# Performance work log

Measured on AMD Instinct MI355X. Metric: run time of the kernel, lower is better.

Reference implementation:

```python
import jax, jax.numpy as jnp
import numpy as np

N_ATOMS = 100_000
N_PAIRS = 6_400_000
CUTOFF = 5.0
CUTON = 4.0


def setup_inputs() -> dict:
    key = jax.random.key(0)
    k = jax.random.split(key, 4)
    atomic_numbers = jax.random.uniform(k[0], (N_ATOMS,), jnp.float32, 1.0, 94.0)
    displacements = jax.random.normal(k[1], (N_PAIRS, 3), jnp.float32) * 2.0
    idx_i = jnp.sort(jax.random.randint(k[2], (N_PAIRS,), 0, N_ATOMS, jnp.int32))
    idx_j = jax.random.randint(k[3], (N_PAIRS,), 0, N_ATOMS, jnp.int32)
    atom_mask = jnp.ones((N_ATOMS,), jnp.float32)
    batch_segments = jnp.zeros((N_ATOMS,), jnp.int32)
    batch_mask = jnp.ones((N_PAIRS,), jnp.float32)
    # ZBL parameters (non-trainable constants from setup())
    a_coefficient = jnp.asarray(0.8854, jnp.float32)
    a_exponent = jnp.asarray(0.23, jnp.float32)
    phi_coefficients = jnp.array([0.18175, 0.50986, 0.28022, 0.02817], jnp.float32)
    phi_exponents = jnp.array([3.1998, 0.94229, 0.4029, 0.20162], jnp.float32)
    return dict(
        atomic_numbers=atomic_numbers,
        displacements=displacements,
        idx_i=idx_i,
        idx_j=idx_j,
        atom_mask=atom_mask,
        batch_segments=batch_segments,
        batch_mask=batch_mask,
        batch_size=1,
        a_coefficient=a_coefficient,
        a_exponent=a_exponent,
        phi_coefficients=phi_coefficients,
        phi_exponents=phi_exponents,
    )


def _switch_fn(distances):
    # smooth 1 -> 0 switch between CUTON and CUTOFF
    x = (CUTOFF - distances) / (CUTOFF - CUTON)
    poly = ((6.0 * x - 15.0) * x + 10.0) * x ** 3
    return jnp.where(distances < CUTON, 1.0, jnp.where(distances >= CUTOFF, 0.0, poly))


def reference(atomic_numbers, displacements, idx_i, idx_j, atom_mask,
              batch_segments, batch_mask, batch_size,
              a_coefficient, a_exponent, phi_coefficients, phi_exponents):
    distances = jnp.maximum(jnp.linalg.norm(displacements, axis=-1), 1e-10)  # [E]
    switch_off = _switch_fn(distances)

    za = jnp.power(atomic_numbers, jnp.abs(a_exponent))  # [N]
    denominator = jnp.maximum(za[idx_i] + za[idx_j], 1e-10)  # [E]
    a_ij = jnp.abs(a_coefficient) / denominator
    arguments = distances / a_ij  # [E]

    coefficients = jax.nn.softmax(jnp.abs(phi_coefficients))  # [4]
    exponents = jnp.abs(phi_exponents)  # [4]
    log_terms = -exponents[None, :] * arguments[:, None]  # [E,4]
    max_log = jnp.max(log_terms, axis=1, keepdims=True)
    # NOTE: faithful to the original -- max_log is never added back
    phi = jnp.sum(coefficients[None, :] * jnp.exp(log_terms - max_log), axis=1)  # [E]

    log_repulsion = (jnp.log(0.5)
                     + jnp.log(atomic_numbers[idx_i])
                     + jnp.log(atomic_numbers[idx_j])
                     - jnp.log(distances)
                     + jnp.log(jnp.maximum(phi, 1e-30))
                     + jnp.log(jnp.maximum(switch_off, 1e-30)))
    repulsion = jnp.exp(log_repulsion) * batch_mask  # [E]

    Erep = jax.ops.segment_sum(repulsion, segment_ids=idx_i,
                               num_segments=atomic_numbers.shape[0])  # [N]
    Erep = Erep * atom_mask
    return Erep[..., None, None, None]
```

## Files before the change

kernel.cpp:

```cpp
#include <hip/hip_runtime.h>
#include <math.h>

#define LOG2E 1.4426950408889634f


__global__ __launch_bounds__(256) void zbl_prep_kernel(
    const float* __restrict__ z, const float* __restrict__ a_coef,
    const float* __restrict__ a_exp, const float* __restrict__ phi_c,
    const float* __restrict__ phi_e, float2* __restrict__ tab,
    float* __restrict__ out, float* __restrict__ consts, int n_atoms) {
  int n = blockIdx.x * blockDim.x + threadIdx.x;
  if (n < n_atoms) {
    float zi = z[n];
    float ae = fabsf(a_exp[0]);
    float za = __builtin_amdgcn_exp2f(ae * __builtin_amdgcn_logf(zi));
    tab[n] = make_float2(zi, za);
    out[n] = 0.0f;
  }
  if (blockIdx.x == 0 && threadIdx.x == 0) {
    float c[4], e2[4];
    float m = -1e30f;
    for (int k = 0; k < 4; ++k) { c[k] = fabsf(phi_c[k]); m = fmaxf(m, c[k]); }
    float s = 0.0f;
    for (int k = 0; k < 4; ++k) { c[k] = expf(c[k] - m); s += c[k]; }
    for (int k = 0; k < 4; ++k) c[k] /= s;
    int kmin = 0;
    for (int k = 0; k < 4; ++k) {
      e2[k] = fabsf(phi_e[k]) * LOG2E;
      if (e2[k] < e2[kmin]) kmin = k;
    }
    float inv_a = 1.0f / fabsf(a_coef[0]);
    consts[0] = c[kmin];
    int p = 1;
    for (int k = 0; k < 4; ++k) {
      if (k != kmin) {
        consts[p] = c[k];
        consts[3 + p] = (e2[k] - e2[kmin]) * inv_a;
        ++p;
      }
    }
  }
}

__global__ __launch_bounds__(256) void zbl_edge_kernel(
    const float* __restrict__ disp, const int* __restrict__ idx_i,
    const int* __restrict__ idx_j, const float* __restrict__ bmask,
    const float2* __restrict__ tab, const float* __restrict__ consts,
    const float* __restrict__ amask, float* __restrict__ out, int n_edges) {
  const int lane = threadIdx.x & 63;
  const long wave = (long)blockIdx.x * (blockDim.x >> 6) + (threadIdx.x >> 6);
  const long base = wave * 256;

  const float c0 = consts[0], c1 = consts[1], c2 = consts[2], c3 = consts[3];
  const float dd1 = consts[4], dd2 = consts[5], dd3 = consts[6];

  #pragma unroll
  for (int c = 0; c < 4; ++c) {
    const long e = base + (long)(c << 6) + lane;
    int key = -1;
    float v = 0.0f;
    if (e < (long)n_edges) {
      const int i = idx_i[e];
      const int j = idx_j[e];
      const float dx = disp[3 * e + 0];
      const float dy = disp[3 * e + 1];
      const float dz = disp[3 * e + 2];
      float n2 = fmaxf(dx * dx + dy * dy + dz * dz, 1e-20f);
      float r = __builtin_amdgcn_rsqf(n2);
      float d = n2 * r;
      float x = 5.0f - d;
      float poly = ((6.0f * x - 15.0f) * x + 10.0f) * x * x * x;
      float sw = (d < 4.0f) ? 1.0f : ((d >= 5.0f) ? 0.0f : poly);
      float2 ti = tab[i];
      float2 tj = tab[j];
      float q = d * fmaxf(ti.y + tj.y, 1e-10f);
      float phi = c0 + c1 * __builtin_amdgcn_exp2f(-dd1 * q)
                     + c2 * __builtin_amdgcn_exp2f(-dd2 * q)
                     + c3 * __builtin_amdgcn_exp2f(-dd3 * q);
      v = 0.5f * ti.x * tj.x * r * fmaxf(phi, 1e-30f) *
          fmaxf(sw, 1e-30f) * bmask[e];
      key = i;
    }

    #pragma unroll
    for (int off = 1; off < 64; off <<= 1) {
      float v2 = __shfl_down(v, off, 64);
      int k2 = __shfl_down(key, off, 64);
      if (lane + off < 64 && k2 == key) v += v2;
    }
    int kup = __shfl_up(key, 1, 64);
    if (key >= 0 && (lane == 0 || kup != key))
      atomicAdd(&out[key], v * amask[key]);
  }
}

extern "C" void kernel_launch(void* const* d_in, const int* in_sizes, int n_in,
                              void* d_out, int out_size, void* d_ws,
                              size_t ws_size, hipStream_t stream) {
  const float* atomic_numbers = (const float*)d_in[0];
  const float* disp           = (const float*)d_in[1];
  const int*   idx_i          = (const int*)d_in[2];
  const int*   idx_j          = (const int*)d_in[3];
  const float* atom_mask      = (const float*)d_in[4];
  const float* bmask          = (const float*)d_in[6];
  const float* a_coef         = (const float*)d_in[8];
  const float* a_exp          = (const float*)d_in[9];
  const float* phi_c          = (const float*)d_in[10];
  const float* phi_e          = (const float*)d_in[11];

  int n_atoms = in_sizes[0];
  int n_edges = in_sizes[2];

  float* out = (float*)d_out;
  float2* tab = (float2*)d_ws;
  float* consts = (float*)((char*)d_ws + (size_t)n_atoms * sizeof(float2));

  int atom_blocks = (n_atoms + 255) / 256;
  long waves = ((long)n_edges + 255) / 256;
  int edge_blocks = (int)((waves + 3) / 4);

  zbl_prep_kernel<<<atom_blocks, 256, 0, stream>>>(
      atomic_numbers, a_coef, a_exp, phi_c, phi_e, tab, out, consts, n_atoms);
  zbl_edge_kernel<<<edge_blocks, 256, 0, stream>>>(
      disp, idx_i, idx_j, bmask, tab, consts, atom_mask, out, n_edges);
}
```

Measured before the change: 53.58 us.

## Vectorize edge loads and aggregate segment sums in shared-memory slots

```diff
diff --git a/kernel.cpp b/kernel.cpp
--- a/kernel.cpp
+++ b/kernel.cpp
@@ -2,6 +2,8 @@
 #include <math.h>
 
 #define LOG2E 1.4426950408889634f
+#define NSLOT 512
+#define EPB   1024
 
 
 __global__ __launch_bounds__(256) void zbl_prep_kernel(
@@ -42,55 +44,101 @@
   }
 }
 
+__device__ __forceinline__ void zbl_edge_compute(
+    float dx, float dy, float dz, int i, int j, float bm,
+    const float2* __restrict__ tab, float c0, float c1, float c2, float c3,
+    float dd1, float dd2, float dd3, int& kk, float& vv) {
+  float n2 = fmaxf(dx * dx + dy * dy + dz * dz, 1e-20f);
+  float r = __builtin_amdgcn_rsqf(n2);
+  float d = n2 * r;
+  float x = 5.0f - d;
+  float poly = ((6.0f * x - 15.0f) * x + 10.0f) * x * x * x;
+  float sw = (d < 4.0f) ? 1.0f : ((d >= 5.0f) ? 0.0f : poly);
+  float2 ti = tab[i];
+  float2 tj = tab[j];
+  float q = d * fmaxf(ti.y + tj.y, 1e-10f);
+  float phi = c0 + c1 * __builtin_amdgcn_exp2f(-dd1 * q)
+                 + c2 * __builtin_amdgcn_exp2f(-dd2 * q)
+                 + c3 * __builtin_amdgcn_exp2f(-dd3 * q);
+  vv = 0.5f * ti.x * tj.x * r * fmaxf(phi, 1e-30f) * fmaxf(sw, 1e-30f) * bm;
+  kk = i;
+}
+
 __global__ __launch_bounds__(256) void zbl_edge_kernel(
     const float* __restrict__ disp, const int* __restrict__ idx_i,
     const int* __restrict__ idx_j, const float* __restrict__ bmask,
     const float2* __restrict__ tab, const float* __restrict__ consts,
     const float* __restrict__ amask, float* __restrict__ out, int n_edges) {
-  const int lane = threadIdx.x & 63;
-  const long wave = (long)blockIdx.x * (blockDim.x >> 6) + (threadIdx.x >> 6);
-  const long base = wave * 256;
+  __shared__ float acc[NSLOT];
+  const int t = threadIdx.x;
+  const long block_base = (long)blockIdx.x * EPB;
 
+  acc[t] = 0.0f;
+  acc[t + 256] = 0.0f;
+
+  const int key_base = idx_i[block_base];
   const float c0 = consts[0], c1 = consts[1], c2 = consts[2], c3 = consts[3];
   const float dd1 = consts[4], dd2 = consts[5], dd3 = consts[6];
 
+  const long L = (long)blockIdx.x * 256 + t;
+  const long e0 = L * 4;
+
+  int k[4] = {-1, -1, -1, -1};
+  float v[4] = {0.f, 0.f, 0.f, 0.f};
+
+  if (e0 + 3 < (long)n_edges) {
+    const float4* d4 = (const float4*)disp;
+    float4 A = d4[3 * L], B = d4[3 * L + 1], Cc = d4[3 * L + 2];
+    int4 I = ((const int4*)idx_i)[L];
+    int4 J = ((const int4*)idx_j)[L];
+    float4 BM = ((const float4*)bmask)[L];
+    zbl_edge_compute(A.x, A.y, A.z, I.x, J.x, BM.x, tab, c0, c1, c2, c3, dd1, dd2, dd3, k[0], v[0]);
+    zbl_edge_compute(A.w, B.x, B.y, I.y, J.y, BM.y, tab, c0, c1, c2, c3, dd1, dd2, dd3, k[1], v[1]);
+    zbl_edge_compute(B.z, B.w, Cc.x, I.z, J.z, BM.z, tab, c0, c1, c2, c3, dd1, dd2, dd3, k[2], v[2]);
+    zbl_edge_compute(Cc.y, Cc.z, Cc.w, I.w, J.w, BM.w, tab, c0, c1, c2, c3, dd1, dd2, dd3, k[3], v[3]);
+  } else {
+    #pragma unroll
+    for (int m = 0; m < 4; ++m) {
+      const long e = e0 + m;
+      if (e < (long)n_edges)
+        zbl_edge_compute(disp[3 * e], disp[3 * e + 1], disp[3 * e + 2],
+                         idx_i[e], idx_j[e], bmask[e], tab, c0, c1, c2, c3,
+                         dd1, dd2, dd3, k[m], v[m]);
+    }
+  }
+
+  __syncthreads();
+
+  auto flush = [&](int key, float s) {
+    if (key < 0) return;
+    int slot = key - key_base;
+    if ((unsigned)slot < (unsigned)NSLOT) atomicAdd(&acc[slot], s);
+    else atomicAdd(&out[key], s * amask[key]);
+  };
+
+  int cur = k[0];
+  float s = v[0];
   #pragma unroll
-  for (int c = 0; c < 4; ++c) {
-    const long e = base + (long)(c << 6) + lane;
-    int key = -1;
-    float v = 0.0f;
-    if (e < (long)n_edges) {
-      const int i = idx_i[e];
-      const int j = idx_j[e];
-      const float dx = disp[3 * e + 0];
-      const float dy = disp[3 * e + 1];
-      const float dz = disp[3 * e + 2];
-      float n2 = fmaxf(dx * dx + dy * dy + dz * dz, 1e-20f);
-      float r = __builtin_amdgcn_rsqf(n2);
-      float d = n2 * r;
-      float x = 5.0f - d;
-      float poly = ((6.0f * x - 15.0f) * x + 10.0f) * x * x * x;
-      float sw = (d < 4.0f) ? 1.0f : ((d >= 5.0f) ? 0.0f : poly);
-      float2 ti = tab[i];
-      float2 tj = tab[j];
-      float q = d * fmaxf(ti.y + tj.y, 1e-10f);
-      float phi = c0 + c1 * __builtin_amdgcn_exp2f(-dd1 * q)
-                     + c2 * __builtin_amdgcn_exp2f(-dd2 * q)
-                     + c3 * __builtin_amdgcn_exp2f(-dd3 * q);
-      v = 0.5f * ti.x * tj.x * r * fmaxf(phi, 1e-30f) *
-          fmaxf(sw, 1e-30f) * bmask[e];
-      key = i;
+  for (int m = 1; m < 4; ++m) {
+    if (k[m] == cur) {
+      s += v[m];
+    } else {
+      flush(cur, s);
+      cur = k[m];
+      s = v[m];
     }
+  }
+  flush(cur, s);
 
-    #pragma unroll
-    for (int off = 1; off < 64; off <<= 1) {
-      float v2 = __shfl_down(v, off, 64);
-      int k2 = __shfl_down(key, off, 64);
-      if (lane + off < 64 && k2 == key) v += v2;
+  __syncthreads();
+
+  #pragma unroll
+  for (int s2 = 0; s2 < NSLOT; s2 += 256) {
+    float val = acc[t + s2];
+    if (val != 0.0f) {
+      int a = key_base + t + s2;
+      atomicAdd(&out[a], val * amask[a]);
     }
-    int kup = __shfl_up(key, 1, 64);
-    if (key >= 0 && (lane == 0 || kup != key))
-      atomicAdd(&out[key], v * amask[key]);
   }
 }
 
@@ -116,8 +164,7 @@
   float* consts = (float*)((char*)d_ws + (size_t)n_atoms * sizeof(float2));
 
   int atom_blocks = (n_atoms + 255) / 256;
-  long waves = ((long)n_edges + 255) / 256;
-  int edge_blocks = (int)((waves + 3) / 4);
+  int edge_blocks = (int)(((long)n_edges + EPB - 1) / EPB);
 
   zbl_prep_kernel<<<atom_blocks, 256, 0, stream>>>(
       atomic_numbers, a_coef, a_exp, phi_c, phi_e, tab, out, consts, n_atoms);
```

Result: faster. 47.43 us (median of 2 runs) (-11.5%).

## Fuse prep into edge kernel with shared-memory segment accumulation per block

Applied to the files above, without the earlier changes.

```diff
diff --git a/kernel.cpp b/kernel.cpp
--- a/kernel.cpp
+++ b/kernel.cpp
@@ -2,95 +2,151 @@
 #include <math.h>
 
 #define LOG2E 1.4426950408889634f
+#define NSLOT 512
+#define EPT   8
+#define EPB   (256 * EPT)
 
+__global__ __launch_bounds__(256, 6) void zbl_fused_kernel(
+    const float* __restrict__ z, const float* __restrict__ amask,
+    const float* __restrict__ disp, const int* __restrict__ idx_i,
+    const int* __restrict__ idx_j, const float* __restrict__ bmask,
+    const float* __restrict__ a_coef, const float* __restrict__ a_exp,
+    const float* __restrict__ phi_c, const float* __restrict__ phi_e,
+    float* __restrict__ out, int n_edges, int n_atoms) {
+  __shared__ float za_s[NSLOT];
+  __shared__ float acc[NSLOT];
+  const int t = threadIdx.x;
+  const long bb = (long)blockIdx.x * EPB;
+  const long Q = (long)blockIdx.x * 256 + t;
+  const long e0 = Q * (long)EPT;
 
-__global__ __launch_bounds__(256) void zbl_prep_kernel(
-    const float* __restrict__ z, const float* __restrict__ a_coef,
-    const float* __restrict__ a_exp, const float* __restrict__ phi_c,
-    const float* __restrict__ phi_e, float2* __restrict__ tab,
-    float* __restrict__ out, float* __restrict__ consts, int n_atoms) {
-  int n = blockIdx.x * blockDim.x + threadIdx.x;
-  if (n < n_atoms) {
-    float zi = z[n];
-    float ae = fabsf(a_exp[0]);
-    float za = __builtin_amdgcn_exp2f(ae * __builtin_amdgcn_logf(zi));
-    tab[n] = make_float2(zi, za);
-    out[n] = 0.0f;
+  const float ae = fabsf(a_exp[0]);
+  const float inv_a = 1.0f / fabsf(a_coef[0]);
+  float cc0 = fabsf(phi_c[0]), cc1 = fabsf(phi_c[1]);
+  float cc2 = fabsf(phi_c[2]), cc3 = fabsf(phi_c[3]);
+  {
+    float mx = fmaxf(fmaxf(cc0, cc1), fmaxf(cc2, cc3));
+    cc0 = expf(cc0 - mx); cc1 = expf(cc1 - mx);
+    cc2 = expf(cc2 - mx); cc3 = expf(cc3 - mx);
+    float inv_s = 1.0f / (cc0 + cc1 + cc2 + cc3);
+    cc0 *= inv_s; cc1 *= inv_s; cc2 *= inv_s; cc3 *= inv_s;
   }
-  if (blockIdx.x == 0 && threadIdx.x == 0) {
-    float c[4], e2[4];
-    float m = -1e30f;
-    for (int k = 0; k < 4; ++k) { c[k] = fabsf(phi_c[k]); m = fmaxf(m, c[k]); }
-    float s = 0.0f;
-    for (int k = 0; k < 4; ++k) { c[k] = expf(c[k] - m); s += c[k]; }
-    for (int k = 0; k < 4; ++k) c[k] /= s;
-    int kmin = 0;
-    for (int k = 0; k < 4; ++k) {
-      e2[k] = fabsf(phi_e[k]) * LOG2E;
-      if (e2[k] < e2[kmin]) kmin = k;
-    }
-    float inv_a = 1.0f / fabsf(a_coef[0]);
-    consts[0] = c[kmin];
-    int p = 1;
-    for (int k = 0; k < 4; ++k) {
-      if (k != kmin) {
-        consts[p] = c[k];
-        consts[3 + p] = (e2[k] - e2[kmin]) * inv_a;
-        ++p;
+  float q0 = fabsf(phi_e[0]) * LOG2E, q1 = fabsf(phi_e[1]) * LOG2E;
+  float q2 = fabsf(phi_e[2]) * LOG2E, q3 = fabsf(phi_e[3]) * LOG2E;
+  const float emin = fminf(fminf(q0, q1), fminf(q2, q3));
+  const float dd0 = (q0 - emin) * inv_a, dd1 = (q1 - emin) * inv_a;
+  const float dd2 = (q2 - emin) * inv_a, dd3 = (q3 - emin) * inv_a;
+
+  const int key_base = idx_i[bb];
+  const int a0 = min(key_base + t, n_atoms - 1);
+  const int a1 = min(key_base + t + 256, n_atoms - 1);
+  const float zw0 = z[a0], zw1 = z[a1];
+  const float am0 = amask[a0], am1 = amask[a1];
+
+  int kk[EPT];
+  float dx[EPT], dy[EPT], dz[EPT], bm[EPT], zj[EPT];
+  #pragma unroll
+  for (int m = 0; m < EPT; ++m) { kk[m] = -1; dx[m] = dy[m] = dz[m] = bm[m] = 0.f; zj[m] = 1.f; }
+
+  if (e0 + (EPT - 1) < (long)n_edges) {
+    int4 I0 = ((const int4*)idx_i)[2 * Q];
+    int4 I1 = ((const int4*)idx_i)[2 * Q + 1];
+    int4 J0 = ((const int4*)idx_j)[2 * Q];
+    int4 J1 = ((const int4*)idx_j)[2 * Q + 1];
+    const float4* d4 = (const float4*)disp;
+    float4 D0 = d4[6 * Q + 0], D1 = d4[6 * Q + 1], D2 = d4[6 * Q + 2];
+    float4 D3 = d4[6 * Q + 3], D4 = d4[6 * Q + 4], D5 = d4[6 * Q + 5];
+    float4 B0 = ((const float4*)bmask)[2 * Q];
+    float4 B1 = ((const float4*)bmask)[2 * Q + 1];
+    zj[0] = z[J0.x]; zj[1] = z[J0.y]; zj[2] = z[J0.z]; zj[3] = z[J0.w];
+    zj[4] = z[J1.x]; zj[5] = z[J1.y]; zj[6] = z[J1.z]; zj[7] = z[J1.w];
+    kk[0] = I0.x; kk[1] = I0.y; kk[2] = I0.z; kk[3] = I0.w;
+    kk[4] = I1.x; kk[5] = I1.y; kk[6] = I1.z; kk[7] = I1.w;
+    dx[0] = D0.x; dy[0] = D0.y; dz[0] = D0.z;
+    dx[1] = D0.w; dy[1] = D1.x; dz[1] = D1.y;
+    dx[2] = D1.z; dy[2] = D1.w; dz[2] = D2.x;
+    dx[3] = D2.y; dy[3] = D2.z; dz[3] = D2.w;
+    dx[4] = D3.x; dy[4] = D3.y; dz[4] = D3.z;
+    dx[5] = D3.w; dy[5] = D4.x; dz[5] = D4.y;
+    dx[6] = D4.z; dy[6] = D4.w; dz[6] = D5.x;
+    dx[7] = D5.y; dy[7] = D5.z; dz[7] = D5.w;
+    bm[0] = B0.x; bm[1] = B0.y; bm[2] = B0.z; bm[3] = B0.w;
+    bm[4] = B1.x; bm[5] = B1.y; bm[6] = B1.z; bm[7] = B1.w;
+  } else {
+    #pragma unroll
+    for (int m = 0; m < EPT; ++m) {
+      const long e = e0 + m;
+      if (e < (long)n_edges) {
+        kk[m] = idx_i[e];
+        zj[m] = z[idx_j[e]];
+        dx[m] = disp[3 * e]; dy[m] = disp[3 * e + 1]; dz[m] = disp[3 * e + 2];
+        bm[m] = bmask[e];
       }
     }
   }
-}
 
-__global__ __launch_bounds__(256) void zbl_edge_kernel(
-    const float* __restrict__ disp, const int* __restrict__ idx_i,
-    const int* __restrict__ idx_j, const float* __restrict__ bmask,
-    const float2* __restrict__ tab, const float* __restrict__ consts,
-    const float* __restrict__ amask, float* __restrict__ out, int n_edges) {
-  const int lane = threadIdx.x & 63;
-  const long wave = (long)blockIdx.x * (blockDim.x >> 6) + (threadIdx.x >> 6);
-  const long base = wave * 256;
+  acc[t] = 0.0f;
+  acc[t + 256] = 0.0f;
+  za_s[t] = __builtin_amdgcn_exp2f(ae * __builtin_amdgcn_logf(zw0));
+  za_s[t + 256] = __builtin_amdgcn_exp2f(ae * __builtin_amdgcn_logf(zw1));
+  const float fi0 = 0.5f * zw0 * am0;
+  const float fi1 = 0.5f * zw1 * am1;
+  __syncthreads();
 
-  const float c0 = consts[0], c1 = consts[1], c2 = consts[2], c3 = consts[3];
-  const float dd1 = consts[4], dd2 = consts[5], dd3 = consts[6];
+  float vv[EPT];
+  #pragma unroll
+  for (int m = 0; m < EPT; ++m) {
+    float za_i;
+    {
+      int s = kk[m] - key_base;
+      if ((unsigned)s < (unsigned)NSLOT) za_i = za_s[s];
+      else if (kk[m] >= 0)
+        za_i = __builtin_amdgcn_exp2f(ae * __builtin_amdgcn_logf(z[kk[m]]));
+      else za_i = 0.0f;
+    }
+    float n2 = fmaxf(dx[m] * dx[m] + dy[m] * dy[m] + dz[m] * dz[m], 1e-20f);
+    float r = __builtin_amdgcn_rsqf(n2);
+    float d = n2 * r;
+    float x = 5.0f - d;
+    float poly = ((6.0f * x - 15.0f) * x + 10.0f) * x * x * x;
+    float sw = (d < 4.0f) ? 1.0f : ((d >= 5.0f) ? 0.0f : poly);
+    float zaj = __builtin_amdgcn_exp2f(ae * __builtin_amdgcn_logf(zj[m]));
+    float qq = d * fmaxf(za_i + zaj, 1e-10f);
+    float phi = cc0 * __builtin_amdgcn_exp2f(-dd0 * qq)
+              + cc1 * __builtin_amdgcn_exp2f(-dd1 * qq)
+              + cc2 * __builtin_amdgcn_exp2f(-dd2 * qq)
+              + cc3 * __builtin_amdgcn_exp2f(-dd3 * qq);
+    vv[m] = zj[m] * r * fmaxf(phi, 1e-30f) * fmaxf(sw, 1e-30f) * bm[m];
+  }
 
-  #pragma unroll
-  for (int c = 0; c < 4; ++c) {
-    const long e = base + (long)(c << 6) + lane;
-    int key = -1;
-    float v = 0.0f;
-    if (e < (long)n_edges) {
-      const int i = idx_i[e];
-      const int j = idx_j[e];
-      const float dx = disp[3 * e + 0];
-      const float dy = disp[3 * e + 1];
-      const float dz = disp[3 * e + 2];
-      float n2 = fmaxf(dx * dx + dy * dy + dz * dz, 1e-20f);
-      float r = __builtin_amdgcn_rsqf(n2);
-      float d = n2 * r;
-      float x = 5.0f - d;
-      float poly = ((6.0f * x - 15.0f) * x + 10.0f) * x * x * x;
-      float sw = (d < 4.0f) ? 1.0f : ((d >= 5.0f) ? 0.0f : poly);
-      float2 ti = tab[i];
-      float2 tj = tab[j];
-      float q = d * fmaxf(ti.y + tj.y, 1e-10f);
-      float phi = c0 + c1 * __builtin_amdgcn_exp2f(-dd1 * q)
-                     + c2 * __builtin_amdgcn_exp2f(-dd2 * q)
-                     + c3 * __builtin_amdgcn_exp2f(-dd3 * q);
-      v = 0.5f * ti.x * tj.x * r * fmaxf(phi, 1e-30f) *
-          fmaxf(sw, 1e-30f) * bmask[e];
-      key = i;
+  auto flush = [&](int key, float s) {
+    if (key < 0) return;
+    int slot = key - key_base;
+    if ((unsigned)slot < (unsigned)NSLOT) {
+      atomicAdd(&acc[slot], s);
+    } else {
+      atomicAdd(&out[key], s * 0.5f * z[key] * amask[key]);
     }
+  };
 
+  {
+    int cur = kk[0];
+    float s = vv[0];
     #pragma unroll
-    for (int off = 1; off < 64; off <<= 1) {
-      float v2 = __shfl_down(v, off, 64);
-      int k2 = __shfl_down(key, off, 64);
-      if (lane + off < 64 && k2 == key) v += v2;
+    for (int m = 1; m < EPT; ++m) {
+      if (kk[m] == cur) s += vv[m];
+      else { flush(cur, s); cur = kk[m]; s = vv[m]; }
     }
-    int kup = __shfl_up(key, 1, 64);
-    if (key >= 0 && (lane == 0 || kup != key))
-      atomicAdd(&out[key], v * amask[key]);
+    flush(cur, s);
+  }
+
+  __syncthreads();
+
+  {
+    float val = acc[t];
+    if (val != 0.0f) atomicAdd(&out[key_base + t], val * fi0);
+    val = acc[t + 256];
+    if (val != 0.0f) atomicAdd(&out[key_base + t + 256], val * fi1);
   }
 }
 
@@ -112,15 +168,11 @@
   int n_edges = in_sizes[2];
 
   float* out = (float*)d_out;
-  float2* tab = (float2*)d_ws;
-  float* consts = (float*)((char*)d_ws + (size_t)n_atoms * sizeof(float2));
 
-  int atom_blocks = (n_atoms + 255) / 256;
-  long waves = ((long)n_edges + 255) / 256;
-  int edge_blocks = (int)((waves + 3) / 4);
+  hipMemsetAsync(out, 0, (size_t)out_size * sizeof(float), stream);
 
-  zbl_prep_kernel<<<atom_blocks, 256, 0, stream>>>(
-      atomic_numbers, a_coef, a_exp, phi_c, phi_e, tab, out, consts, n_atoms);
-  zbl_edge_kernel<<<edge_blocks, 256, 0, stream>>>(
-      disp, idx_i, idx_j, bmask, tab, consts, atom_mask, out, n_edges);
+  int edge_blocks = (int)(((long)n_edges + EPB - 1) / EPB);
+  zbl_fused_kernel<<<edge_blocks, 256, 0, stream>>>(
+      atomic_numbers, atom_mask, disp, idx_i, idx_j, bmask, a_coef, a_exp,
+      phi_c, phi_e, out, n_edges, n_atoms);
 }
```

Result: faster. 47.57 us (-11.2%).
